# Kernel optimization log

Measured on AMD Instinct MI355X. Metric: run time of the kernel, lower is better.

Reference implementation:

```python
import jax, jax.numpy as jnp
import numpy as np

B, S, D, H = 2, 2048, 512, 8
HD = D // H
DFF = 4 * D
EPS_LN = 1e-5
EPS_ATTN = 1e-8


def layernorm(x, w, b):
    mu = jnp.mean(x, axis=-1, keepdims=True)
    var = jnp.var(x, axis=-1, keepdims=True)
    return (x - mu) * jax.lax.rsqrt(var + EPS_LN) * w + b


def masked_attention(q_src, v_src, wq, bq, wk, bk, wv, bv, wo, bo, M):
    # q_src/v_src: (B,S,D); M: (B,S,S)
    Bs, Ss, _ = q_src.shape
    Q = (q_src @ wq + bq).reshape(Bs, Ss, H, HD)
    K = (q_src @ wk + bk).reshape(Bs, Ss, H, HD)
    V = (v_src @ wv + bv).reshape(Bs, Ss, H, HD)
    scale = HD ** -0.5
    scores = jnp.einsum('bqhd,bkhd->bhqk', Q, K) * scale
    Mh = M[:, None, :, :]                      # (B,1,S,S) broadcast over heads
    scores = scores * Mh
    A = jax.nn.softmax(scores, axis=-1)
    A = A * Mh                                 # re-mask post-softmax
    A = A / (jnp.sum(jnp.abs(A), axis=-1, keepdims=True) + EPS_ATTN)  # L1 renorm
    out = jnp.einsum('bhqk,bkhd->bqhd', A, V).reshape(Bs, Ss, D)
    return out @ wo + bo


def ffn(x, w1, b1, w2, b2):
    h = jax.nn.gelu(x @ w1 + b1, approximate=False)
    return x + (h @ w2 + b2)                   # FeedForward(num_layers=2) includes residual


def setup_inputs() -> dict:
    key = jax.random.key(0)
    ks = iter(jax.random.split(key, 64))
    nrm = lambda shape, s=0.02: jax.random.normal(next(ks), shape, jnp.float32) * s
    d = {
        'gene_emb': jax.random.normal(next(ks), (B, S, D), jnp.float32),
        'expr_emb': jax.random.normal(next(ks), (B, S, D), jnp.float32),
        'M': jax.random.uniform(next(ks), (B, S, S), jnp.float32),
    }
    # gene attention params (weights stored (in,out))
    for p in ['g_wq', 'g_wk', 'g_wv', 'g_wo']:
        d[p] = nrm((D, D))
    for p in ['g_bq', 'g_bk', 'g_bv', 'g_bo']:
        d[p] = jnp.zeros((D,), jnp.float32)
    # expr attention params (fused proj 2D->D)
    d['e_wf'] = nrm((2 * D, D)); d['e_bf'] = jnp.zeros((D,), jnp.float32)
    for p in ['e_wq', 'e_wk', 'e_wv', 'e_wo']:
        d[p] = nrm((D, D))
    for p in ['e_bq', 'e_bk', 'e_bv', 'e_bo']:
        d[p] = jnp.zeros((D,), jnp.float32)
    # layernorms
    for p in ['ln_g1_w', 'ln_g2_w', 'ln_e1_w', 'ln_e2_w']:
        d[p] = jnp.ones((D,), jnp.float32)
    for p in ['ln_g1_b', 'ln_g2_b', 'ln_e1_b', 'ln_e2_b']:
        d[p] = jnp.zeros((D,), jnp.float32)
    # FFNs
    d['fg_w1'] = nrm((D, DFF)); d['fg_b1'] = jnp.zeros((DFF,), jnp.float32)
    d['fg_w2'] = nrm((DFF, D)); d['fg_b2'] = jnp.zeros((D,), jnp.float32)
    d['fe_w1'] = nrm((D, DFF)); d['fe_b1'] = jnp.zeros((DFF,), jnp.float32)
    d['fe_w2'] = nrm((DFF, D)); d['fe_b2'] = jnp.zeros((D,), jnp.float32)
    return d


def reference(gene_emb, expr_emb, M,
              g_wq, g_bq, g_wk, g_bk, g_wv, g_bv, g_wo, g_bo,
              e_wf, e_bf, e_wq, e_bq, e_wk, e_bk, e_wv, e_bv, e_wo, e_bo,
              ln_g1_w, ln_g1_b, ln_g2_w, ln_g2_b,
              ln_e1_w, ln_e1_b, ln_e2_w, ln_e2_b,
              fg_w1, fg_b1, fg_w2, fg_b2,
              fe_w1, fe_b1, fe_w2, fe_b2):
    # ----- gene branch -----
    xg = layernorm(gene_emb, ln_g1_w, ln_g1_b)
    attn_g = masked_attention(xg, xg, g_wq, g_bq, g_wk, g_bk, g_wv, g_bv, g_wo, g_bo, M)
    x = gene_emb + attn_g
    x_ln = layernorm(x, ln_g2_w, ln_g2_b)
    out_gene = x + ffn(x_ln, fg_w1, fg_b1, fg_w2, fg_b2)
    # ----- expression branch -----
    y_n = layernorm(expr_emb, ln_e1_w, ln_e1_b)
    fused = jnp.concatenate([gene_emb, y_n], axis=-1) @ e_wf + e_bf
    attn_e = masked_attention(fused, y_n, e_wq, e_bq, e_wk, e_bk, e_wv, e_bv, e_wo, e_bo, M)
    y = expr_emb + attn_e
    y_ln = layernorm(y, ln_e2_w, ln_e2_b)
    out_expr = y + ffn(y_ln, fe_w1, fe_b1, fe_w2, fe_b2)
    return (out_gene, out_expr)
```

## Files before the change

kernel.cpp:

```cpp
#include <hip/hip_runtime.h>
#include <math.h>

#define S_LEN 2048
#define DMODEL 512
#define NROWS 4096
#define NHEAD 8
#define HDIM 64
#define LOG2E 1.4426950408889634f

typedef __attribute__((ext_vector_type(8))) __bf16 bf16x8;
typedef __attribute__((ext_vector_type(4))) float f32x4;

__device__ inline float bf2f(unsigned short h) {
    unsigned u = ((unsigned)h) << 16;
    return __builtin_bit_cast(float, u);
}
__device__ inline unsigned short f2bf(float f) {
    unsigned u = __builtin_bit_cast(unsigned, f);
    return (unsigned short)((u + 0x7fffu + ((u >> 16) & 1u)) >> 16);
}

__device__ inline void gl_lds16(const unsigned short* g, unsigned short* l) {
    __builtin_amdgcn_global_load_lds(
        (const __attribute__((address_space(1))) void*)g,
        (__attribute__((address_space(3))) void*)l, 16, 0, 0);
}

__global__ __launch_bounds__(256) void prep_all(
    const float* g_wq, const float* g_wk, const float* g_wv, const float* g_wo,
    const float* e_wq, const float* e_wk, const float* e_wv, const float* e_wo,
    const float* e_wf, const float* fg_w1, const float* fe_w1,
    const float* fg_w2, const float* fe_w2,
    const float* g_bq, const float* g_bk, const float* g_bv,
    const float* e_bq, const float* e_bk,
    unsigned short* __restrict__ wbase, float* __restrict__ biasg,
    float* __restrict__ biase)
{
    const int id = blockIdx.x;
    const int tid = threadIdx.x;
    if (id >= 6656) {
        int t = id - 6656;
        if (t < 6) {
            int i = t * 256 + tid;
            biasg[i] = (i < 512) ? g_bq[i] : (i < 1024) ? g_bk[i - 512] : g_bv[i - 1024];
        } else {
            int i = (t - 6) * 256 + tid;
            biase[i] = (i < 512) ? e_bq[i] : e_bk[i - 512];
        }
        return;
    }
    const float* W; unsigned short* Wt; int K, Mo, bx, by;
    if (id < 2048) {
        const float* srcs[8] = {g_wq, g_wk, g_wv, g_wo, e_wq, e_wk, e_wv, e_wo};
        int m = id >> 8, t = id & 255;
        W = srcs[m]; Wt = wbase + (size_t)m * 512 * 512; K = 512; Mo = 512;
        bx = (t & 15) * 32; by = (t >> 4) * 32;
    } else if (id < 2560) {
        int t = id - 2048;
        W = e_wf; Wt = wbase + 8 * 512 * 512; K = 1024; Mo = 512;
        bx = (t & 15) * 32; by = (t >> 4) * 32;
    } else if (id < 4608) {
        int t = id - 2560; int which = t >> 10; t &= 1023;
        W = which ? fe_w1 : fg_w1;
        Wt = wbase + 8 * 512 * 512 + 1024 * 512 + (size_t)which * 512 * 2048;
        K = 512; Mo = 2048;
        bx = (t & 63) * 32; by = (t >> 6) * 32;
    } else {
        int t = id - 4608; int which = t >> 10; t &= 1023;
        W = which ? fe_w2 : fg_w2;
        Wt = wbase + 8 * 512 * 512 + 1024 * 512 + 2 * 512 * 2048 + (size_t)which * 2048 * 512;
        K = 2048; Mo = 512;
        bx = (t & 15) * 32; by = (t >> 4) * 32;
    }
    __shared__ float tsh[32][33];
    const int tx = tid & 31, ty = tid >> 5;
    #pragma unroll
    for (int r = 0; r < 4; ++r)
        tsh[ty + 8 * r][tx] = W[(size_t)(by + ty + 8 * r) * Mo + bx + tx];
    __syncthreads();
    #pragma unroll
    for (int r = 0; r < 4; ++r)
        Wt[(size_t)(bx + ty + 8 * r) * K + by + tx] = f2bf(tsh[tx][ty + 8 * r]);
}

__global__ __launch_bounds__(256) void ln_front(
    const float* __restrict__ gene, const float* __restrict__ expr,
    const float* __restrict__ gw, const float* __restrict__ gb,
    const float* __restrict__ ew, const float* __restrict__ eb,
    unsigned short* __restrict__ yg,
    unsigned short* __restrict__ ycat)
{
    __shared__ float red[16];
    const int row = blockIdx.x, t = threadIdx.x;
    const float* gr = gene + (size_t)row * DMODEL;
    const float* er = expr + (size_t)row * DMODEL;
    float g0 = gr[t], g1 = gr[t + 256];
    float e0 = er[t], e1 = er[t + 256];
    float sg = g0 + g1, sqg = g0 * g0 + g1 * g1;
    float se = e0 + e1, sqe = e0 * e0 + e1 * e1;
    #pragma unroll
    for (int o = 32; o > 0; o >>= 1) {
        sg += __shfl_down(sg, o);  sqg += __shfl_down(sqg, o);
        se += __shfl_down(se, o);  sqe += __shfl_down(sqe, o);
    }
    int wid = t >> 6, lane = t & 63;
    if (lane == 0) {
        red[wid] = sg; red[4 + wid] = sqg; red[8 + wid] = se; red[12 + wid] = sqe;
    }
    __syncthreads();
    float mg  = (red[0] + red[1] + red[2] + red[3]) * (1.0f / 512.0f);
    float qg_ = (red[4] + red[5] + red[6] + red[7]) * (1.0f / 512.0f);
    float me  = (red[8] + red[9] + red[10] + red[11]) * (1.0f / 512.0f);
    float qe_ = (red[12] + red[13] + red[14] + red[15]) * (1.0f / 512.0f);
    float rg = rsqrtf(qg_ - mg * mg + 1e-5f);
    float re = rsqrtf(qe_ - me * me + 1e-5f);
    yg[(size_t)row * 512 + t]         = f2bf((g0 - mg) * rg * gw[t] + gb[t]);
    yg[(size_t)row * 512 + t + 256]   = f2bf((g1 - mg) * rg * gw[t + 256] + gb[t + 256]);
    unsigned short* yr = ycat + (size_t)row * 1024;
    yr[t]             = f2bf(g0);
    yr[t + 256]       = f2bf(g1);
    yr[512 + t]       = f2bf((e0 - me) * re * ew[t] + eb[t]);
    yr[512 + t + 256] = f2bf((e1 - me) * re * ew[t + 256] + eb[t + 256]);
}

__global__ __launch_bounds__(256) void ln_kernel(
    const float* __restrict__ x, const float* __restrict__ w,
    const float* __restrict__ b, unsigned short* __restrict__ y, int ostride)
{
    __shared__ float red[8];
    const int row = blockIdx.x;
    const float* xr = x + (size_t)row * DMODEL;
    const int t = threadIdx.x;
    float v0 = xr[t];
    float v1 = xr[t + 256];
    float s  = v0 + v1;
    float sq = v0 * v0 + v1 * v1;
    #pragma unroll
    for (int o = 32; o > 0; o >>= 1) {
        s  += __shfl_down(s, o);
        sq += __shfl_down(sq, o);
    }
    int wid = t >> 6, lane = t & 63;
    if (lane == 0) { red[wid] = s; red[4 + wid] = sq; }
    __syncthreads();
    float mean = (red[0] + red[1] + red[2] + red[3]) * (1.0f / 512.0f);
    float msq  = (red[4] + red[5] + red[6] + red[7]) * (1.0f / 512.0f);
    float var  = msq - mean * mean;
    float rs   = rsqrtf(var + 1e-5f);
    y[(size_t)row * ostride + t]       = f2bf((v0 - mean) * rs * w[t] + b[t]);
    y[(size_t)row * ostride + t + 256] = f2bf((v1 - mean) * rs * w[t + 256] + b[t + 256]);
}

__global__ __launch_bounds__(256) void vtrans(
    const unsigned short* __restrict__ V, int ldv, unsigned short* __restrict__ Vt)
{
    __shared__ unsigned short t[64][72];
    const int s0 = blockIdx.x * 64, h = blockIdx.y, b = blockIdx.z;
    const int tid = threadIdx.x;
    {
        const int r = tid >> 2, c = (tid & 3) * 16;
        const unsigned short* src = V + (size_t)(b * S_LEN + s0 + r) * ldv + h * 64 + c;
        *(int4*)&t[r][c]     = *(const int4*)(src);
        *(int4*)&t[r][c + 8] = *(const int4*)(src + 8);
    }
    __syncthreads();
    {
        const int d = tid >> 2, s = (tid & 3) * 16;
        unsigned short* dst = Vt + ((size_t)((b * 8 + h) * 64 + d)) * S_LEN + s0 + s;
        unsigned short tmp[16];
        #pragma unroll
        for (int e = 0; e < 16; ++e) tmp[e] = t[s + e][d];
        *(int4*)dst       = *(int4*)&tmp[0];
        *(int4*)(dst + 8) = *(int4*)&tmp[8];
    }
}

__global__ __launch_bounds__(256) void gemm_mfma(
    const unsigned short* __restrict__ A, int lda,
    const unsigned short* __restrict__ Bt,
    const float* __restrict__ bias,
    const float* __restrict__ R1,
    const unsigned short* __restrict__ R2,
    float* __restrict__ Cf, unsigned short* __restrict__ Cb,
    int K, int Mo, int dogelu)
{
    __shared__ __align__(16) unsigned short As[3][128 * 32];
    __shared__ __align__(16) unsigned short Bs[3][128 * 32];
    const int tid = threadIdx.x;
    const int wave = tid >> 6, lane = tid & 63;
    const int wr = wave >> 1, wc = wave & 1;
    const int row0 = blockIdx.y * 128, col0 = blockIdx.x * 128;
    const int l15 = lane & 15, q = lane >> 4;

    f32x4 acc[4][4];
    const f32x4 zz = {0.f, 0.f, 0.f, 0.f};
    #pragma unroll
    for (int i = 0; i < 4; ++i)
        #pragma unroll
        for (int j = 0; j < 4; ++j) acc[i][j] = zz;

    const int nk = K >> 5;
    auto stage = [&](int t, int buf) {
        const int k0 = t * 32;
        #pragma unroll
        for (int r = 0; r < 2; ++r) {
            int idx = r * 256 + tid;
            int row = idx >> 2, kc = idx & 3;
            gl_lds16(&A[(size_t)(row0 + row) * lda + k0 + kc * 8],
                     &As[buf][(size_t)(r * 256 + wave * 64) * 8]);
            gl_lds16(&Bt[(size_t)(col0 + row) * K + k0 + kc * 8],
                     &Bs[buf][(size_t)(r * 256 + wave * 64) * 8]);
        }
    };
    stage(0, 0);
    if (nk > 1) stage(1, 1);

    int cur = 0, nx2 = 2;
    for (int t = 0; t < nk; ++t) {
        if (t + 1 < nk) asm volatile("s_waitcnt vmcnt(4)" ::: "memory");
        else            asm volatile("s_waitcnt vmcnt(0)" ::: "memory");
        __builtin_amdgcn_s_barrier();
        if (t + 2 < nk) stage(t + 2, nx2);

        bf16x8 af[4], bfr[4];
        #pragma unroll
        for (int fi = 0; fi < 4; ++fi)
            af[fi] = *(const bf16x8*)&As[cur][(wr * 64 + fi * 16 + l15) * 32 + q * 8];
        #pragma unroll
        for (int fj = 0; fj < 4; ++fj)
            bfr[fj] = *(const bf16x8*)&Bs[cur][(wc * 64 + fj * 16 + l15) * 32 + q * 8];
        #pragma unroll
        for (int fi = 0; fi < 4; ++fi)
            #pragma unroll
            for (int fj = 0; fj < 4; ++fj)
                acc[fi][fj] = __builtin_amdgcn_mfma_f32_16x16x32_bf16(
                    af[fi], bfr[fj], acc[fi][fj], 0, 0, 0);

        cur = (cur == 2) ? 0 : cur + 1;
        nx2 = (nx2 == 2) ? 0 : nx2 + 1;
    }

    #pragma unroll
    for (int fi = 0; fi < 4; ++fi) {
        #pragma unroll
        for (int reg = 0; reg < 4; ++reg) {
            int row = row0 + wr * 64 + fi * 16 + q * 4 + reg;
            #pragma unroll
            for (int fj = 0; fj < 4; ++fj) {
                int col = col0 + wc * 64 + fj * 16 + l15;
                float v = acc[fi][fj][reg] + bias[col];
                if (dogelu) v = 0.5f * v * (1.0f + erff(v * 0.70710678118654752f));
                size_t off = (size_t)row * Mo + col;
                if (R1) v += R1[off];
                if (R2) v += bf2f(R2[off]);
                if (Cb) Cb[off] = f2bf(v);
                else    Cf[off] = v;
            }
        }
    }
}

__global__ __launch_bounds__(256) void gemm_mfma64(
    const unsigned short* __restrict__ A, int lda,
    const unsigned short* __restrict__ Bt,
    const float* __restrict__ bias,
    const float* __restrict__ R1,
    const unsigned short* __restrict__ R2,
    float* __restrict__ Cf, unsigned short* __restrict__ Cb,
    int K, int Mo, int dogelu)
{
    __shared__ __align__(16) unsigned short As[3][64 * 64];
    __shared__ __align__(16) unsigned short Bs[3][64 * 64];
    const int tid = threadIdx.x;
    const int wave = tid >> 6, lane = tid & 63;
    const int row0 = blockIdx.y * 64, col0 = blockIdx.x * 64;
    const int l15 = lane & 15, q = lane >> 4;

    f32x4 acc[4];
    const f32x4 zz = {0.f, 0.f, 0.f, 0.f};
    #pragma unroll
    for (int j = 0; j < 4; ++j) acc[j] = zz;

    const int nk = K >> 6;
    auto stage = [&](int t, int buf) {
        const int k0 = t * 64;
        #pragma unroll
        for (int r = 0; r < 2; ++r) {
            int idx = r * 256 + tid;
            int row = idx >> 3;
            int kc  = (idx & 7) ^ (row & 7);
            gl_lds16(&A[(size_t)(row0 + row) * lda + k0 + kc * 8],
                     &As[buf][(size_t)(r * 256 + wave * 64) * 8]);
            gl_lds16(&Bt[(size_t)(col0 + row) * K + k0 + kc * 8],
                     &Bs[buf][(size_t)(r * 256 + wave * 64) * 8]);
        }
    };
    stage(0, 0);
    if (nk > 1) stage(1, 1);

    int cur = 0, nx2 = 2;
    for (int t = 0; t < nk; ++t) {
        if (t + 1 < nk) asm volatile("s_waitcnt vmcnt(4)" ::: "memory");
        else            asm volatile("s_waitcnt vmcnt(0)" ::: "memory");
        __builtin_amdgcn_s_barrier();
        if (t + 2 < nk) stage(t + 2, nx2);

        #pragma unroll
        for (int ks = 0; ks < 2; ++ks) {
            const int cx = ((ks * 4 + q) ^ (l15 & 7)) * 8;
            bf16x8 af = *(const bf16x8*)&As[cur][(wave * 16 + l15) * 64 + cx];
            bf16x8 bfr[4];
            #pragma unroll
            for (int fj = 0; fj < 4; ++fj)
                bfr[fj] = *(const bf16x8*)&Bs[cur][(fj * 16 + l15) * 64 + cx];
            #pragma unroll
            for (int fj = 0; fj < 4; ++fj)
                acc[fj] = __builtin_amdgcn_mfma_f32_16x16x32_bf16(af, bfr[fj], acc[fj], 0, 0, 0);
        }

        cur = (cur == 2) ? 0 : cur + 1;
        nx2 = (nx2 == 2) ? 0 : nx2 + 1;
    }

    #pragma unroll
    for (int reg = 0; reg < 4; ++reg) {
        int row = row0 + wave * 16 + q * 4 + reg;
        #pragma unroll
        for (int fj = 0; fj < 4; ++fj) {
            int col = col0 + fj * 16 + l15;
            float v = acc[fj][reg] + bias[col];
            if (dogelu) v = 0.5f * v * (1.0f + erff(v * 0.70710678118654752f));
            size_t off = (size_t)row * Mo + col;
            if (R1) v += R1[off];
            if (R2) v += bf2f(R2[off]);
            if (Cb) Cb[off] = f2bf(v);
            else    Cf[off] = v;
        }
    }
}

__global__ __launch_bounds__(256, 4) void attn_mfma(
    const unsigned short* __restrict__ Q, int ldq,
    const unsigned short* __restrict__ Kp, int ldk,
    const unsigned short* __restrict__ Vt,
    const float* __restrict__ M,
    unsigned short* __restrict__ O)
{
    __shared__ __align__(16) unsigned short Ks[64 * 72];
    __shared__ __align__(16) unsigned short Vs[64 * 72];
    __shared__ __align__(16) unsigned short Ps_all[4][16 * 72];

    const int bh = blockIdx.y, b = bh >> 3, h = bh & 7;
    const int q0 = blockIdx.x * 64;
    const int tid = threadIdx.x, wave = tid >> 6, lane = tid & 63;
    const int l15 = lane & 15, quad = lane >> 4;
    const int iRow = q0 + wave * 16 + l15;

    unsigned short* Ps = &Ps_all[wave][0];

    bf16x8 qf[2];
    {
        const unsigned short* qp = Q + (size_t)(b * S_LEN + iRow) * ldq + h * HDIM + quad * 8;
        #pragma unroll
        for (int ks = 0; ks < 2; ++ks) {
            union { bf16x8 v; unsigned short u[8]; } tq;
            tq.v = *(const bf16x8*)(qp + ks * 32);
            #pragma unroll
            for (int e = 0; e < 8; ++e)
                tq.u[e] = f2bf(bf2f(tq.u[e]) * (0.125f * LOG2E));
            qf[ks] = tq.v;
        }
    }

    const int srow = tid >> 3;
    const int scol = (tid & 7) * 8;
    const unsigned short* kg = Kp + ((size_t)b * S_LEN) * ldk + h * HDIM + scol;
    const unsigned short* vg = Vt + ((size_t)bh * 64 + srow) * S_LEN + scol;
    const float* mrow = M + ((size_t)b * S_LEN + iRow) * S_LEN + quad * 4;

    float rm = -INFINITY, rZ = 0.f, rZm = 0.f;
    f32x4 oacc[4];
    const f32x4 zz = {0.f, 0.f, 0.f, 0.f};
    #pragma unroll
    for (int dt = 0; dt < 4; ++dt) oacc[dt] = zz;

    int4 kv0 = *(const int4*)(kg + (size_t)srow * ldk);
    int4 kv1 = *(const int4*)(kg + (size_t)(srow + 32) * ldk);
    int4 vv0 = *(const int4*)(vg);
    int4 vv1 = *(const int4*)(vg + 32 * S_LEN);
    float4 m4[4], m4n[4];
    #pragma unroll
    for (int jt = 0; jt < 4; ++jt)
        m4[jt] = *(const float4*)(mrow + jt * 16);
    *(int4*)&Ks[srow * 72 + scol]        = kv0;
    *(int4*)&Ks[(srow + 32) * 72 + scol] = kv1;
    *(int4*)&Vs[srow * 72 + scol]        = vv0;
    *(int4*)&Vs[(srow + 32) * 72 + scol] = vv1;
    __syncthreads();

    for (int k0 = 0; k0 < S_LEN; k0 += 64) {
        const bool more = (k0 + 64 < S_LEN);
        if (more) {
            kv0 = *(const int4*)(kg + (size_t)(k0 + 64 + srow) * ldk);
            kv1 = *(const int4*)(kg + (size_t)(k0 + 64 + srow + 32) * ldk);
            vv0 = *(const int4*)(vg + k0 + 64);
            vv1 = *(const int4*)(vg + 32 * S_LEN + k0 + 64);
            #pragma unroll
            for (int jt = 0; jt < 4; ++jt)
                m4n[jt] = *(const float4*)(mrow + k0 + 64 + jt * 16);
        }

        f32x4 sacc[4];
        #pragma unroll
        for (int jt = 0; jt < 4; ++jt) sacc[jt] = zz;
        __builtin_amdgcn_s_setprio(1);
        #pragma unroll
        for (int jt = 0; jt < 4; ++jt) {
            bf16x8 kf0 = *(const bf16x8*)&Ks[(jt * 16 + l15) * 72 + quad * 8];
            bf16x8 kf1 = *(const bf16x8*)&Ks[(jt * 16 + l15) * 72 + 32 + quad * 8];
            sacc[jt] = __builtin_amdgcn_mfma_f32_16x16x32_bf16(kf0, qf[0], sacc[jt], 0, 0, 0);
            sacc[jt] = __builtin_amdgcn_mfma_f32_16x16x32_bf16(kf1, qf[1], sacc[jt], 0, 0, 0);
        }
        __builtin_amdgcn_s_setprio(0);

        float mxj[4];
        #pragma unroll
        for (int jt = 0; jt < 4; ++jt) {
            float mm[4] = {m4[jt].x, m4[jt].y, m4[jt].z, m4[jt].w};
            #pragma unroll
            for (int r = 0; r < 4; ++r)
                sacc[jt][r] = sacc[jt][r] * mm[r];
            mxj[jt] = fmaxf(fmaxf(sacc[jt][0], sacc[jt][1]),
                            fmaxf(sacc[jt][2], sacc[jt][3]));
        }
        float mx = fmaxf(fmaxf(mxj[0], mxj[1]), fmaxf(mxj[2], mxj[3]));
        mx = fmaxf(mx, __shfl_xor(mx, 16));
        mx = fmaxf(mx, __shfl_xor(mx, 32));
        if (!__all(mx <= rm + 8.0f)) {
            float mn = fmaxf(rm, mx);
            float al = __builtin_amdgcn_exp2f(rm - mn);
            rm = mn; rZ *= al; rZm *= al;
            #pragma unroll
            for (int dt = 0; dt < 4; ++dt)
                #pragma unroll
                for (int r = 0; r < 4; ++r) oacc[dt][r] *= al;
        }

        float z = 0.f, zm = 0.f;
        #pragma unroll
        for (int jt = 0; jt < 4; ++jt) {
            float mm[4] = {m4[jt].x, m4[jt].y, m4[jt].z, m4[jt].w};
            float pv[4];
            #pragma unroll
            for (int r = 0; r < 4; ++r) {
                float e = __builtin_amdgcn_exp2f(sacc[jt][r] - rm);
                float pm = e * mm[r];
                z += e; zm += pm; pv[r] = pm;
            }
            unsigned lo, hi;
            asm("v_cvt_pk_bf16_f32 %0, %1, %2" : "=v"(lo) : "v"(pv[0]), "v"(pv[1]));
            asm("v_cvt_pk_bf16_f32 %0, %1, %2" : "=v"(hi) : "v"(pv[2]), "v"(pv[3]));
            uint2 pk; pk.x = lo; pk.y = hi;
            *(uint2*)&Ps[l15 * 72 + jt * 16 + quad * 4] = pk;
        }
        rZ += z; rZm += zm;

        bf16x8 pf0 = *(const bf16x8*)&Ps[l15 * 72 + quad * 8];
        bf16x8 pf1 = *(const bf16x8*)&Ps[l15 * 72 + 32 + quad * 8];
        __builtin_amdgcn_s_setprio(1);
        #pragma unroll
        for (int dt = 0; dt < 4; ++dt) {
            bf16x8 vf0 = *(const bf16x8*)&Vs[(dt * 16 + l15) * 72 + quad * 8];
            bf16x8 vf1 = *(const bf16x8*)&Vs[(dt * 16 + l15) * 72 + 32 + quad * 8];
            oacc[dt] = __builtin_amdgcn_mfma_f32_16x16x32_bf16(vf0, pf0, oacc[dt], 0, 0, 0);
            oacc[dt] = __builtin_amdgcn_mfma_f32_16x16x32_bf16(vf1, pf1, oacc[dt], 0, 0, 0);
        }
        __builtin_amdgcn_s_setprio(0);

        if (more) {
            __syncthreads();
            *(int4*)&Ks[srow * 72 + scol]        = kv0;
            *(int4*)&Ks[(srow + 32) * 72 + scol] = kv1;
            *(int4*)&Vs[srow * 72 + scol]        = vv0;
            *(int4*)&Vs[(srow + 32) * 72 + scol] = vv1;
            __syncthreads();
            #pragma unroll
            for (int jt = 0; jt < 4; ++jt) m4[jt] = m4n[jt];
        }
    }

    rZ  += __shfl_xor(rZ, 16);  rZ  += __shfl_xor(rZ, 32);
    rZm += __shfl_xor(rZm, 16); rZm += __shfl_xor(rZm, 32);
    float inv = 1.0f / (rZm + 1e-8f * rZ);

    unsigned short* op = O + (size_t)(b * S_LEN + iRow) * DMODEL + h * HDIM;
    #pragma unroll
    for (int dt = 0; dt < 4; ++dt) {
        float o0 = oacc[dt][0] * inv, o1 = oacc[dt][1] * inv;
        float o2 = oacc[dt][2] * inv, o3 = oacc[dt][3] * inv;
        unsigned lo, hi;
        asm("v_cvt_pk_bf16_f32 %0, %1, %2" : "=v"(lo) : "v"(o0), "v"(o1));
        asm("v_cvt_pk_bf16_f32 %0, %1, %2" : "=v"(hi) : "v"(o2), "v"(o3));
        uint2 o2v; o2v.x = lo; o2v.y = hi;
        *(uint2*)(op + dt * 16 + quad * 4) = o2v;
    }
}

extern "C" void kernel_launch(void* const* d_in, const int* in_sizes, int n_in,
                              void* d_out, int out_size, void* d_ws, size_t ws_size,
                              hipStream_t stream)
{
    const float* gene_emb = (const float*)d_in[0];
    const float* expr_emb = (const float*)d_in[1];
    const float* M        = (const float*)d_in[2];
    const float* g_wq = (const float*)d_in[3];
    const float* g_wk = (const float*)d_in[4];
    const float* g_wv = (const float*)d_in[5];
    const float* g_wo = (const float*)d_in[6];
    const float* g_bq = (const float*)d_in[7];
    const float* g_bk = (const float*)d_in[8];
    const float* g_bv = (const float*)d_in[9];
    const float* g_bo = (const float*)d_in[10];
    const float* e_wf = (const float*)d_in[11];
    const float* e_bf = (const float*)d_in[12];
    const float* e_wq = (const float*)d_in[13];
    const float* e_wk = (const float*)d_in[14];
    const float* e_wv = (const float*)d_in[15];
    const float* e_wo = (const float*)d_in[16];
    const float* e_bq = (const float*)d_in[17];
    const float* e_bk = (const float*)d_in[18];
    const float* e_bv = (const float*)d_in[19];
    const float* e_bo = (const float*)d_in[20];
    const float* ln_g1_w = (const float*)d_in[21];
    const float* ln_g2_w = (const float*)d_in[22];
    const float* ln_e1_w = (const float*)d_in[23];
    const float* ln_e2_w = (const float*)d_in[24];
    const float* ln_g1_b = (const float*)d_in[25];
    const float* ln_g2_b = (const float*)d_in[26];
    const float* ln_e1_b = (const float*)d_in[27];
    const float* ln_e2_b = (const float*)d_in[28];
    const float* fg_w1 = (const float*)d_in[29];
    const float* fg_b1 = (const float*)d_in[30];
    const float* fg_w2 = (const float*)d_in[31];
    const float* fg_b2 = (const float*)d_in[32];
    const float* fe_w1 = (const float*)d_in[33];
    const float* fe_b1 = (const float*)d_in[34];
    const float* fe_w2 = (const float*)d_in[35];
    const float* fe_b2 = (const float*)d_in[36];

    float* out_gene = (float*)d_out;
    float* out_expr = out_gene + (size_t)NROWS * DMODEL;

    char* ws = (char*)d_ws;
    const size_t MB1 = 1024 * 1024;
    unsigned short* bufA16  = (unsigned short*)(ws + 0 * MB1);
    unsigned short* bufAt16 = (unsigned short*)(ws + 4 * MB1);
    unsigned short* bufQKV  = (unsigned short*)(ws + 8 * MB1);
    unsigned short* bufQKe  = (unsigned short*)(ws + 8 * MB1);
    unsigned short* bufV16  = (unsigned short*)(ws + 16 * MB1);
    unsigned short* bufVt   = (unsigned short*)(ws + 20 * MB1);
    unsigned short* bufCat  = (unsigned short*)(ws + 24 * MB1);
    float*          bufX    = (float*)(ws + 33 * MB1);
    unsigned short* bufH16  = (unsigned short*)(ws + 8 * MB1);
    char* wp = ws + 41 * MB1;
    unsigned short* sq8    = (unsigned short*)wp;
    unsigned short* gwq_t  = sq8 + 0 * 512 * 512;
    unsigned short* gwo_t  = sq8 + 3 * 512 * 512;
    unsigned short* ewq_t  = sq8 + 4 * 512 * 512;
    unsigned short* ewv_t  = sq8 + 6 * 512 * 512;
    unsigned short* ewo_t  = sq8 + 7 * 512 * 512;
    unsigned short* ewf_t  = sq8 + 8 * 512 * 512;
    unsigned short* ffn1   = ewf_t + 1024 * 512;
    unsigned short* fgw1_t = ffn1;
    unsigned short* few1_t = ffn1 + 512 * 2048;
    unsigned short* ffn2   = few1_t + 512 * 2048;
    unsigned short* fgw2_t = ffn2;
    unsigned short* few2_t = ffn2 + 2048 * 512;
    float* biasg = (float*)(few2_t + 2048 * 512);
    float* biase = biasg + 1536;

    dim3 blk(256);
    dim3 ln_grid(NROWS);
    dim3 g512s(8, 64);
    dim3 g1024(8, 32);
    dim3 g1536(12, 32);
    dim3 g2048(16, 32);
    dim3 attn_grid(S_LEN / 64, 16);
    dim3 vt_grid(S_LEN / 64, NHEAD, 2);

    prep_all<<<dim3(6666), blk, 0, stream>>>(
        g_wq, g_wk, g_wv, g_wo, e_wq, e_wk, e_wv, e_wo,
        e_wf, fg_w1, fe_w1, fg_w2, fe_w2,
        g_bq, g_bk, g_bv, e_bq, e_bk,
        sq8, biasg, biase);

    ln_front<<<ln_grid, blk, 0, stream>>>(
        gene_emb, expr_emb, ln_g1_w, ln_g1_b, ln_e1_w, ln_e1_b, bufA16, bufCat);

    gemm_mfma<<<g1536, blk, 0, stream>>>(bufA16, 512, gwq_t, biasg, nullptr, nullptr, nullptr, bufQKV, 512, 1536, 0);
    vtrans<<<vt_grid, blk, 0, stream>>>(bufQKV + 1024, 1536, bufVt);
    attn_mfma<<<attn_grid, blk, 0, stream>>>(bufQKV, 1536, bufQKV + 512, 1536, bufVt, M, bufAt16);
    gemm_mfma64<<<g512s, blk, 0, stream>>>(bufAt16, 512, gwo_t, g_bo, gene_emb, nullptr, bufX, nullptr, 512, 512, 0);
    ln_kernel<<<ln_grid, blk, 0, stream>>>(bufX, ln_g2_w, ln_g2_b, bufA16, 512);
    gemm_mfma<<<g2048, blk, 0, stream>>>(bufA16, 512, fgw1_t, fg_b1, nullptr, nullptr, nullptr, bufH16, 512, 2048, 1);
    gemm_mfma64<<<g512s, blk, 0, stream>>>(bufH16, 2048, fgw2_t, fg_b2, bufX, bufA16, out_gene, nullptr, 2048, 512, 0);

    gemm_mfma64<<<g512s, blk, 0, stream>>>(bufCat, 1024, ewf_t, e_bf, nullptr, nullptr, nullptr, bufA16, 1024, 512, 0);
    gemm_mfma<<<g1024, blk, 0, stream>>>(bufA16, 512, ewq_t, biase, nullptr, nullptr, nullptr, bufQKe, 512, 1024, 0);
    gemm_mfma64<<<g512s, blk, 0, stream>>>(bufCat + 512, 1024, ewv_t, e_bv, nullptr, nullptr, nullptr, bufV16, 512, 512, 0);
    vtrans<<<vt_grid, blk, 0, stream>>>(bufV16, 512, bufVt);
    attn_mfma<<<attn_grid, blk, 0, stream>>>(bufQKe, 1024, bufQKe + 512, 1024, bufVt, M, bufAt16);
    gemm_mfma64<<<g512s, blk, 0, stream>>>(bufAt16, 512, ewo_t, e_bo, expr_emb, nullptr, bufX, nullptr, 512, 512, 0);
    ln_kernel<<<ln_grid, blk, 0, stream>>>(bufX, ln_e2_w, ln_e2_b, bufA16, 512);
    gemm_mfma<<<g2048, blk, 0, stream>>>(bufA16, 512, few1_t, fe_b1, nullptr, nullptr, nullptr, bufH16, 512, 2048, 1);
    gemm_mfma64<<<g512s, blk, 0, stream>>>(bufH16, 2048, few2_t, fe_b2, bufX, bufA16, out_expr, nullptr, 2048, 512, 0);
}
```

Baseline: 521.2 us.

## Split attention keys across two wave groups and widen GEMM blocks to 512 threads

The attention kernel now runs 512 threads per block. Two groups of four waves each process half of the key sequence with separate K/V shared buffers, and at the end the partial max, sums and outputs are merged through shared memory in split-softmax style. This doubles the waves working on each query tile so more latency is hidden across the long 2048-key loop, at the cost of a merge step, a larger shared footprint, and launch bounds that may cap registers. The 128x128 GEMM also moves to 8 waves, each computing a 64x32 sub-tile, with one load per thread per stage. That gives more waves per tile but halves the per-wave MFMA work per LDS fragment load.

```diff
diff --git a/kernel.cpp b/kernel.cpp
--- a/kernel.cpp
+++ b/kernel.cpp
@@ -175,7 +175,7 @@
     }
 }
 
-__global__ __launch_bounds__(256) void gemm_mfma(
+__global__ __launch_bounds__(512) void gemm_mfma(
     const unsigned short* __restrict__ A, int lda,
     const unsigned short* __restrict__ Bt,
     const float* __restrict__ bias,
@@ -188,51 +188,47 @@
     __shared__ __align__(16) unsigned short Bs[3][128 * 32];
     const int tid = threadIdx.x;
     const int wave = tid >> 6, lane = tid & 63;
-    const int wr = wave >> 1, wc = wave & 1;
+    const int wr = wave >> 2, wc = wave & 3;
     const int row0 = blockIdx.y * 128, col0 = blockIdx.x * 128;
     const int l15 = lane & 15, q = lane >> 4;
 
-    f32x4 acc[4][4];
+    f32x4 acc[4][2];
     const f32x4 zz = {0.f, 0.f, 0.f, 0.f};
     #pragma unroll
     for (int i = 0; i < 4; ++i)
         #pragma unroll
-        for (int j = 0; j < 4; ++j) acc[i][j] = zz;
+        for (int j = 0; j < 2; ++j) acc[i][j] = zz;
 
     const int nk = K >> 5;
     auto stage = [&](int t, int buf) {
         const int k0 = t * 32;
-        #pragma unroll
-        for (int r = 0; r < 2; ++r) {
-            int idx = r * 256 + tid;
-            int row = idx >> 2, kc = idx & 3;
-            gl_lds16(&A[(size_t)(row0 + row) * lda + k0 + kc * 8],
-                     &As[buf][(size_t)(r * 256 + wave * 64) * 8]);
-            gl_lds16(&Bt[(size_t)(col0 + row) * K + k0 + kc * 8],
-                     &Bs[buf][(size_t)(r * 256 + wave * 64) * 8]);
-        }
+        const int row = tid >> 2, kc = tid & 3;
+        gl_lds16(&A[(size_t)(row0 + row) * lda + k0 + kc * 8],
+                 &As[buf][(size_t)(wave * 64) * 8]);
+        gl_lds16(&Bt[(size_t)(col0 + row) * K + k0 + kc * 8],
+                 &Bs[buf][(size_t)(wave * 64) * 8]);
     };
     stage(0, 0);
     if (nk > 1) stage(1, 1);
 
     int cur = 0, nx2 = 2;
     for (int t = 0; t < nk; ++t) {
-        if (t + 1 < nk) asm volatile("s_waitcnt vmcnt(4)" ::: "memory");
+        if (t + 1 < nk) asm volatile("s_waitcnt vmcnt(2)" ::: "memory");
         else            asm volatile("s_waitcnt vmcnt(0)" ::: "memory");
         __builtin_amdgcn_s_barrier();
         if (t + 2 < nk) stage(t + 2, nx2);
 
-        bf16x8 af[4], bfr[4];
+        bf16x8 af[4], bfr[2];
         #pragma unroll
         for (int fi = 0; fi < 4; ++fi)
             af[fi] = *(const bf16x8*)&As[cur][(wr * 64 + fi * 16 + l15) * 32 + q * 8];
         #pragma unroll
-        for (int fj = 0; fj < 4; ++fj)
-            bfr[fj] = *(const bf16x8*)&Bs[cur][(wc * 64 + fj * 16 + l15) * 32 + q * 8];
+        for (int fj = 0; fj < 2; ++fj)
+            bfr[fj] = *(const bf16x8*)&Bs[cur][(wc * 32 + fj * 16 + l15) * 32 + q * 8];
         #pragma unroll
         for (int fi = 0; fi < 4; ++fi)
             #pragma unroll
-            for (int fj = 0; fj < 4; ++fj)
+            for (int fj = 0; fj < 2; ++fj)
                 acc[fi][fj] = __builtin_amdgcn_mfma_f32_16x16x32_bf16(
                     af[fi], bfr[fj], acc[fi][fj], 0, 0, 0);
 
@@ -246,8 +242,8 @@
         for (int reg = 0; reg < 4; ++reg) {
             int row = row0 + wr * 64 + fi * 16 + q * 4 + reg;
             #pragma unroll
-            for (int fj = 0; fj < 4; ++fj) {
-                int col = col0 + wc * 64 + fj * 16 + l15;
+            for (int fj = 0; fj < 2; ++fj) {
+                int col = col0 + wc * 32 + fj * 16 + l15;
                 float v = acc[fi][fj][reg] + bias[col];
                 if (dogelu) v = 0.5f * v * (1.0f + erff(v * 0.70710678118654752f));
                 size_t off = (size_t)row * Mo + col;
@@ -339,24 +335,30 @@
     }
 }
 
-__global__ __launch_bounds__(256, 4) void attn_mfma(
+__global__ __launch_bounds__(512, 4) void attn_mfma(
     const unsigned short* __restrict__ Q, int ldq,
     const unsigned short* __restrict__ Kp, int ldk,
     const unsigned short* __restrict__ Vt,
     const float* __restrict__ M,
     unsigned short* __restrict__ O)
 {
-    __shared__ __align__(16) unsigned short Ks[64 * 72];
-    __shared__ __align__(16) unsigned short Vs[64 * 72];
-    __shared__ __align__(16) unsigned short Ps_all[4][16 * 72];
-
+    __shared__ __align__(16) unsigned short smem[27648];
+
+    const int tid = threadIdx.x;
+    const int grp = tid >> 8;
+    const int gtid = tid & 255;
+    const int wave = tid >> 6;
+    const int wrow = wave & 3;
+    const int lane = tid & 63;
+    const int l15 = lane & 15, quad = lane >> 4;
     const int bh = blockIdx.y, b = bh >> 3, h = bh & 7;
     const int q0 = blockIdx.x * 64;
-    const int tid = threadIdx.x, wave = tid >> 6, lane = tid & 63;
-    const int l15 = lane & 15, quad = lane >> 4;
-    const int iRow = q0 + wave * 16 + l15;
-
-    unsigned short* Ps = &Ps_all[wave][0];
+    const int iRow = q0 + wrow * 16 + l15;
+    const int kBeg = grp * (S_LEN / 2), kEnd = kBeg + (S_LEN / 2);
+
+    unsigned short* Ks = smem + grp * 9216;
+    unsigned short* Vs = Ks + 4608;
+    unsigned short* Ps = smem + 18432 + wave * 1152;
 
     bf16x8 qf[2];
     {
@@ -372,8 +374,8 @@
         }
     }
 
-    const int srow = tid >> 3;
-    const int scol = (tid & 7) * 8;
+    const int srow = gtid >> 3;
+    const int scol = (gtid & 7) * 8;
     const unsigned short* kg = Kp + ((size_t)b * S_LEN) * ldk + h * HDIM + scol;
     const unsigned short* vg = Vt + ((size_t)bh * 64 + srow) * S_LEN + scol;
     const float* mrow = M + ((size_t)b * S_LEN + iRow) * S_LEN + quad * 4;
@@ -384,22 +386,22 @@
     #pragma unroll
     for (int dt = 0; dt < 4; ++dt) oacc[dt] = zz;
 
-    int4 kv0 = *(const int4*)(kg + (size_t)srow * ldk);
-    int4 kv1 = *(const int4*)(kg + (size_t)(srow + 32) * ldk);
-    int4 vv0 = *(const int4*)(vg);
-    int4 vv1 = *(const int4*)(vg + 32 * S_LEN);
+    int4 kv0 = *(const int4*)(kg + (size_t)(kBeg + srow) * ldk);
+    int4 kv1 = *(const int4*)(kg + (size_t)(kBeg + srow + 32) * ldk);
+    int4 vv0 = *(const int4*)(vg + kBeg);
+    int4 vv1 = *(const int4*)(vg + 32 * S_LEN + kBeg);
     float4 m4[4], m4n[4];
     #pragma unroll
     for (int jt = 0; jt < 4; ++jt)
-        m4[jt] = *(const float4*)(mrow + jt * 16);
+        m4[jt] = *(const float4*)(mrow + kBeg + jt * 16);
     *(int4*)&Ks[srow * 72 + scol]        = kv0;
     *(int4*)&Ks[(srow + 32) * 72 + scol] = kv1;
     *(int4*)&Vs[srow * 72 + scol]        = vv0;
     *(int4*)&Vs[(srow + 32) * 72 + scol] = vv1;
     __syncthreads();
 
-    for (int k0 = 0; k0 < S_LEN; k0 += 64) {
-        const bool more = (k0 + 64 < S_LEN);
+    for (int k0 = kBeg; k0 < kEnd; k0 += 64) {
+        const bool more = (k0 + 64 < kEnd);
         if (more) {
             kv0 = *(const int4*)(kg + (size_t)(k0 + 64 + srow) * ldk);
             kv1 = *(const int4*)(kg + (size_t)(k0 + 64 + srow + 32) * ldk);
@@ -489,20 +491,47 @@
         }
     }
 
-    rZ  += __shfl_xor(rZ, 16);  rZ  += __shfl_xor(rZ, 32);
-    rZm += __shfl_xor(rZm, 16); rZm += __shfl_xor(rZm, 32);
-    float inv = 1.0f / (rZm + 1e-8f * rZ);
-
-    unsigned short* op = O + (size_t)(b * S_LEN + iRow) * DMODEL + h * HDIM;
-    #pragma unroll
-    for (int dt = 0; dt < 4; ++dt) {
-        float o0 = oacc[dt][0] * inv, o1 = oacc[dt][1] * inv;
-        float o2 = oacc[dt][2] * inv, o3 = oacc[dt][3] * inv;
-        unsigned lo, hi;
-        asm("v_cvt_pk_bf16_f32 %0, %1, %2" : "=v"(lo) : "v"(o0), "v"(o1));
-        asm("v_cvt_pk_bf16_f32 %0, %1, %2" : "=v"(hi) : "v"(o2), "v"(o3));
-        uint2 o2v; o2v.x = lo; o2v.y = hi;
-        *(uint2*)(op + dt * 16 + quad * 4) = o2v;
+    __syncthreads();
+    float* mO = (float*)smem;
+    float* mS = (float*)((char*)smem + 20480);
+    if (grp == 1) {
+        #pragma unroll
+        for (int dt = 0; dt < 4; ++dt)
+            *(f32x4*)&mO[gtid * 20 + dt * 4] = oacc[dt];
+        mS[gtid * 3 + 0] = rm;
+        mS[gtid * 3 + 1] = rZ;
+        mS[gtid * 3 + 2] = rZm;
+    }
+    __syncthreads();
+    if (grp == 0) {
+        float rm1 = mS[gtid * 3 + 0], rZ1 = mS[gtid * 3 + 1], rZm1 = mS[gtid * 3 + 2];
+        float mstar = fmaxf(rm, rm1);
+        float a0 = __builtin_amdgcn_exp2f(rm - mstar);
+        float a1 = __builtin_amdgcn_exp2f(rm1 - mstar);
+        rZ  = rZ * a0 + rZ1 * a1;
+        rZm = rZm * a0 + rZm1 * a1;
+        #pragma unroll
+        for (int dt = 0; dt < 4; ++dt) {
+            f32x4 o1 = *(const f32x4*)&mO[gtid * 20 + dt * 4];
+            #pragma unroll
+            for (int r = 0; r < 4; ++r)
+                oacc[dt][r] = oacc[dt][r] * a0 + o1[r] * a1;
+        }
+        rZ  += __shfl_xor(rZ, 16);  rZ  += __shfl_xor(rZ, 32);
+        rZm += __shfl_xor(rZm, 16); rZm += __shfl_xor(rZm, 32);
+        float inv = 1.0f / (rZm + 1e-8f * rZ);
+
+        unsigned short* op = O + (size_t)(b * S_LEN + iRow) * DMODEL + h * HDIM;
+        #pragma unroll
+        for (int dt = 0; dt < 4; ++dt) {
+            float o0 = oacc[dt][0] * inv, o1 = oacc[dt][1] * inv;
+            float o2 = oacc[dt][2] * inv, o3 = oacc[dt][3] * inv;
+            unsigned lo, hi;
+            asm("v_cvt_pk_bf16_f32 %0, %1, %2" : "=v"(lo) : "v"(o0), "v"(o1));
+            asm("v_cvt_pk_bf16_f32 %0, %1, %2" : "=v"(hi) : "v"(o2), "v"(o3));
+            uint2 o2v; o2v.x = lo; o2v.y = hi;
+            *(uint2*)(op + dt * 16 + quad * 4) = o2v;
+        }
     }
 }
 
@@ -580,6 +609,7 @@
     float* biase = biasg + 1536;
 
     dim3 blk(256);
+    dim3 blk512(512);
     dim3 ln_grid(NROWS);
     dim3 g512s(8, 64);
     dim3 g1024(8, 32);
@@ -597,21 +627,21 @@
     ln_front<<<ln_grid, blk, 0, stream>>>(
         gene_emb, expr_emb, ln_g1_w, ln_g1_b, ln_e1_w, ln_e1_b, bufA16, bufCat);
 
-    gemm_mfma<<<g1536, blk, 0, stream>>>(bufA16, 512, gwq_t, biasg, nullptr, nullptr, nullptr, bufQKV, 512, 1536, 0);
+    gemm_mfma<<<g1536, blk512, 0, stream>>>(bufA16, 512, gwq_t, biasg, nullptr, nullptr, nullptr, bufQKV, 512, 1536, 0);
     vtrans<<<vt_grid, blk, 0, stream>>>(bufQKV + 1024, 1536, bufVt);
-    attn_mfma<<<attn_grid, blk, 0, stream>>>(bufQKV, 1536, bufQKV + 512, 1536, bufVt, M, bufAt16);
+    attn_mfma<<<attn_grid, blk512, 0, stream>>>(bufQKV, 1536, bufQKV + 512, 1536, bufVt, M, bufAt16);
     gemm_mfma64<<<g512s, blk, 0, stream>>>(bufAt16, 512, gwo_t, g_bo, gene_emb, nullptr, bufX, nullptr, 512, 512, 0);
     ln_kernel<<<ln_grid, blk, 0, stream>>>(bufX, ln_g2_w, ln_g2_b, bufA16, 512);
-    gemm_mfma<<<g2048, blk, 0, stream>>>(bufA16, 512, fgw1_t, fg_b1, nullptr, nullptr, nullptr, bufH16, 512, 2048, 1);
+    gemm_mfma<<<g2048, blk512, 0, stream>>>(bufA16, 512, fgw1_t, fg_b1, nullptr, nullptr, nullptr, bufH16, 512, 2048, 1);
     gemm_mfma64<<<g512s, blk, 0, stream>>>(bufH16, 2048, fgw2_t, fg_b2, bufX, bufA16, out_gene, nullptr, 2048, 512, 0);
 
     gemm_mfma64<<<g512s, blk, 0, stream>>>(bufCat, 1024, ewf_t, e_bf, nullptr, nullptr, nullptr, bufA16, 1024, 512, 0);
-    gemm_mfma<<<g1024, blk, 0, stream>>>(bufA16, 512, ewq_t, biase, nullptr, nullptr, nullptr, bufQKe, 512, 1024, 0);
+    gemm_mfma<<<g1024, blk512, 0, stream>>>(bufA16, 512, ewq_t, biase, nullptr, nullptr, nullptr, bufQKe, 512, 1024, 0);
     gemm_mfma64<<<g512s, blk, 0, stream>>>(bufCat + 512, 1024, ewv_t, e_bv, nullptr, nullptr, nullptr, bufV16, 512, 512, 0);
     vtrans<<<vt_grid, blk, 0, stream>>>(bufV16, 512, bufVt);
-    attn_mfma<<<attn_grid, blk, 0, stream>>>(bufQKe, 1024, bufQKe + 512, 1024, bufVt, M, bufAt16);
+    attn_mfma<<<attn_grid, blk512, 0, stream>>>(bufQKe, 1024, bufQKe + 512, 1024, bufVt, M, bufAt16);
     gemm_mfma64<<<g512s, blk, 0, stream>>>(bufAt16, 512, ewo_t, e_bo, expr_emb, nullptr, bufX, nullptr, 512, 512, 0);
     ln_kernel<<<ln_grid, blk, 0, stream>>>(bufX, ln_e2_w, ln_e2_b, bufA16, 512);
-    gemm_mfma<<<g2048, blk, 0, stream>>>(bufA16, 512, few1_t, fe_b1, nullptr, nullptr, nullptr, bufH16, 512, 2048, 1);
+    gemm_mfma<<<g2048, blk512, 0, stream>>>(bufA16, 512, few1_t, fe_b1, nullptr, nullptr, nullptr, bufH16, 512, 2048, 1);
     gemm_mfma64<<<g512s, blk, 0, stream>>>(bufH16, 2048, few2_t, fe_b2, bufX, bufA16, out_expr, nullptr, 2048, 512, 0);
 }
```

After: 549.7 us. 1.05x slower.
